# Optimization experiments

Measured on AMD Instinct MI355X. Metric: run time of the kernel, lower is better.

The kernel has to match this reference:

```python
import jax, jax.numpy as jnp
import numpy as np
import math

H = 16
D_MODEL = 1024
D_K = D_MODEL // H
B = 4
S = 2048


def setup_inputs() -> dict:
    key = jax.random.key(0)
    ks = jax.random.split(key, 11)
    s_in = 1.0 / math.sqrt(D_MODEL)
    inp = {
        "query": jax.random.normal(ks[0], (B, S, D_MODEL), dtype=jnp.float32),
        "key_": jax.random.normal(ks[1], (B, S, D_MODEL), dtype=jnp.float32),
        "value": jax.random.normal(ks[2], (B, S, D_MODEL), dtype=jnp.float32),
        # stacked per-head projection weights: [h, d_model, d_k]
        "Wq": jax.random.uniform(ks[3], (H, D_MODEL, D_K), jnp.float32, -s_in, s_in),
        "bq": jax.random.uniform(ks[4], (H, D_K), jnp.float32, -s_in, s_in),
        "Wk": jax.random.uniform(ks[5], (H, D_MODEL, D_K), jnp.float32, -s_in, s_in),
        "bk": jax.random.uniform(ks[6], (H, D_K), jnp.float32, -s_in, s_in),
        "Wv": jax.random.uniform(ks[7], (H, D_MODEL, D_K), jnp.float32, -s_in, s_in),
        "bv": jax.random.uniform(ks[8], (H, D_K), jnp.float32, -s_in, s_in),
        "Wo": jax.random.uniform(ks[9], (D_MODEL, D_MODEL), jnp.float32, -s_in, s_in),
        "bo": jax.random.uniform(ks[10], (D_MODEL,), jnp.float32, -s_in, s_in),
    }
    return inp


def reference(query, key_, value, Wq, bq, Wk, bk, Wv, bv, Wo, bo):
    # Per-head projections, batched over heads: [b,s,m] x [h,m,k] -> [b,h,s,k]
    q = jnp.einsum("bsm,hmk->bhsk", query, Wq) + bq[None, :, None, :]
    k = jnp.einsum("bsm,hmk->bhsk", key_, Wk) + bk[None, :, None, :]
    v = jnp.einsum("bsm,hmk->bhsk", value, Wv) + bv[None, :, None, :]
    # scores: q @ k^T -> [b,h,Sq,Sk]
    scores = jnp.einsum("bhqk,bhsk->bhqs", q, k) / jnp.sqrt(jnp.float32(D_K))
    # NOTE: original code softmaxes over dim=1 of the per-head [N,Sq,Sk]
    # tensor, i.e. the QUERY axis (axis=2 here). Mask has no effect
    # (masked_fill result is discarded in the source), so it is omitted.
    attn = jax.nn.softmax(scores, axis=2)
    ctx = jnp.einsum("bhqs,bhsk->bhqk", attn, v)  # [b,h,Sq,d_k]
    # concat heads along last dim (head-major order matches torch.cat)
    ctx = jnp.transpose(ctx, (0, 2, 1, 3)).reshape(B, S, D_MODEL)
    out = ctx @ Wo.T + bo  # final_W; dropout = identity (eval mode)
    return out
```

## Files before the change

### kernel.cpp

```cpp
#include <hip/hip_runtime.h>


#define DEV __device__ __forceinline__

typedef __bf16 bf16x8 __attribute__((ext_vector_type(8)));
typedef float  f32x4  __attribute__((ext_vector_type(4)));

DEV unsigned short f2bf(float f) {
    __bf16 h = (__bf16)f;
    return __builtin_bit_cast(unsigned short, h);
}

DEV bf16x8 ldfrag(const unsigned short* p) {
    return *reinterpret_cast<const bf16x8*>(p);
}

DEV float fast_exp2(float x) {
#if __has_builtin(__builtin_amdgcn_exp2f)
    return __builtin_amdgcn_exp2f(x);
#else
    return exp2f(x);
#endif
}

DEV void gld16(const unsigned short* g, unsigned short* l) {
    __builtin_amdgcn_global_load_lds(
        (__attribute__((address_space(1))) void*)g,
        (__attribute__((address_space(3))) void*)l, 16, 0, 0);
}

#define MFMA(a,b,c) __builtin_amdgcn_mfma_f32_16x16x32_bf16((a),(b),(c),0,0,0)

#define QSCALE 0.18033688011112042f

__global__ __launch_bounds__(256) void wprep(const float* __restrict__ Wq,
                                             const float* __restrict__ Wk,
                                             const float* __restrict__ Wv,
                                             const float* __restrict__ Wo,
                                             unsigned short* __restrict__ Wt,
                                             unsigned short* __restrict__ Wot) {
    int idx = blockIdx.x * 256 + threadIdx.x;
    int which = blockIdx.y;
    if (which == 3) { Wot[idx] = f2bf(Wo[idx]); return; }
    const float* W = (which == 0) ? Wq : (which == 1) ? Wk : Wv;
    int n = idx >> 10, m = idx & 1023;
    int h = n >> 6, k = n & 63;
    Wt[(size_t)which * 1048576 + idx] = f2bf(W[h * 65536 + m * 64 + k]);
}

__global__ __launch_bounds__(256) void xprep(const float* __restrict__ X,
                                             unsigned short* __restrict__ Xb) {
    int idx = (blockIdx.x * 256 + threadIdx.x) * 4;
    float4 f = *(const float4*)&X[idx];
    ushort4 o;
    o.x = f2bf(f.x); o.y = f2bf(f.y); o.z = f2bf(f.z); o.w = f2bf(f.w);
    *(ushort4*)&Xb[idx] = o;
}

__global__ __launch_bounds__(256) void proj_gemm(
        const unsigned short* __restrict__ Xb, const unsigned short* __restrict__ Bt,
        const float* __restrict__ bias, unsigned short* __restrict__ O,
        unsigned short* __restrict__ Vt, int z) {
    const int tid = threadIdx.x;
    const int bm = blockIdx.x, bn = blockIdx.y;

    __shared__ __align__(16) unsigned short As[128 * 32];
    __shared__ __align__(16) unsigned short Bs[128 * 32];

    const int lane = tid & 63, wid = tid >> 6;
    const int l16 = lane & 15, quad = lane >> 4;
    const int wm = wid & 1, wn = wid >> 1;

    const unsigned short* ga =
        Xb + (size_t)(bm * 128 + wid * 32 + (lane >> 2)) * 1024 + (lane & 3) * 8;
    const unsigned short* gb =
        Bt + (size_t)(bn * 128 + wid * 32 + (lane >> 2)) * 1024 + (lane & 3) * 8;
    unsigned short* la = &As[wid * 32 * 32];
    unsigned short* lb = &Bs[wid * 32 * 32];

    f32x4 acc[4][4] = {};
    for (int kt = 0; kt < 32; ++kt) {
        __syncthreads();
        const int k0 = kt * 32;
        gld16(ga + k0, la);
        gld16(ga + k0 + 16 * 1024, la + 16 * 32);
        gld16(gb + k0, lb);
        gld16(gb + k0 + 16 * 1024, lb + 16 * 32);
        __syncthreads();
        bf16x8 af[4], bfr[4];
#pragma unroll
        for (int mi = 0; mi < 4; ++mi)
            af[mi] = ldfrag(&As[(wm * 64 + mi * 16 + l16) * 32 + quad * 8]);
#pragma unroll
        for (int ni = 0; ni < 4; ++ni)
            bfr[ni] = ldfrag(&Bs[(wn * 64 + ni * 16 + l16) * 32 + quad * 8]);
#pragma unroll
        for (int mi = 0; mi < 4; ++mi)
#pragma unroll
            for (int ni = 0; ni < 4; ++ni)
                acc[mi][ni] = MFMA(af[mi], bfr[ni], acc[mi][ni]);
    }

#pragma unroll
    for (int mi = 0; mi < 4; ++mi)
#pragma unroll
        for (int ni = 0; ni < 4; ++ni)
#pragma unroll
            for (int r = 0; r < 4; ++r) {
                int row = bm * 128 + wm * 64 + mi * 16 + quad * 4 + r;
                int col = bn * 128 + wn * 64 + ni * 16 + l16;
                float v = acc[mi][ni][r] + bias[col];
                if (z == 0) v *= QSCALE;
                int b = row >> 11, s = row & 2047;
                int h = col >> 6, k = col & 63;
                unsigned short o = f2bf(v);
                if (z == 2) {
                    Vt[(size_t)((b * 16 + h) * 64 + k) * 2048 + s] = o;
                } else {
                    O[(size_t)((b * 16 + h) * 2048 + s) * 64 + k] = o;
                }
            }
}

__global__ __launch_bounds__(256) void colsum_vscale(
        const unsigned short* __restrict__ Qh, const unsigned short* __restrict__ Kh,
        unsigned short* __restrict__ Vt) {
    const int tid = threadIdx.x;
    const int st = blockIdx.x, bh = blockIdx.y;
    const unsigned short* Qb = Qh + (size_t)bh * 2048 * 64;
    const unsigned short* Kb = Kh + (size_t)bh * 2048 * 64;

    __shared__ __align__(16) unsigned short Qs[2 * 128 * 32];
    __shared__ float Dtmp[2][128];
    __shared__ float Dsh[128];

    const int lane = tid & 63, wid = tid >> 6;
    const int l16 = lane & 15, quad = lane >> 4;
    const int wm = wid & 1, wn = wid >> 1;

    bf16x8 kf[2][4];
#pragma unroll
    for (int ks = 0; ks < 2; ++ks)
#pragma unroll
        for (int ni = 0; ni < 4; ++ni)
            kf[ks][ni] = ldfrag(&Kb[(size_t)(st * 128 + wn * 64 + ni * 16 + l16) * 64 +
                                    ks * 32 + quad * 8]);

    const unsigned short* gq =
        Qb + (size_t)(wid * 32 + (lane >> 2)) * 64 + (lane & 3) * 8;

    float psum[4] = {0.f, 0.f, 0.f, 0.f};
    for (int q0 = 0; q0 < 2048; q0 += 128) {
        __syncthreads();
#pragma unroll
        for (int ks = 0; ks < 2; ++ks) {
            gld16(gq + (size_t)q0 * 64 + ks * 32, &Qs[ks * 4096 + wid * 32 * 32]);
            gld16(gq + (size_t)(q0 + 16) * 64 + ks * 32,
                  &Qs[ks * 4096 + (wid * 32 + 16) * 32]);
        }
        __syncthreads();
        f32x4 acc[4][4] = {};
#pragma unroll
        for (int ks = 0; ks < 2; ++ks) {
            bf16x8 af[4];
#pragma unroll
            for (int mi = 0; mi < 4; ++mi)
                af[mi] = ldfrag(&Qs[ks * 4096 + (wm * 64 + mi * 16 + l16) * 32 + quad * 8]);
#pragma unroll
            for (int mi = 0; mi < 4; ++mi)
#pragma unroll
                for (int ni = 0; ni < 4; ++ni)
                    acc[mi][ni] = MFMA(af[mi], kf[ks][ni], acc[mi][ni]);
        }
#pragma unroll
        for (int ni = 0; ni < 4; ++ni) {
            float d = 0.f;
#pragma unroll
            for (int mi = 0; mi < 4; ++mi)
#pragma unroll
                for (int r = 0; r < 4; ++r)
                    d += fast_exp2(acc[mi][ni][r]);
            psum[ni] += d;
        }
    }
#pragma unroll
    for (int ni = 0; ni < 4; ++ni) {
        float v = psum[ni];
        v += __shfl_xor(v, 16, 64);
        v += __shfl_xor(v, 32, 64);
        if (quad == 0) Dtmp[wm][wn * 64 + ni * 16 + l16] = v;
    }
    __syncthreads();
    if (tid < 128) Dsh[tid] = 1.0f / (Dtmp[0][tid] + Dtmp[1][tid]);
    __syncthreads();

    const int k = tid >> 2, c = tid & 3;
    unsigned short* vrow = Vt + ((size_t)bh * 64 + k) * 2048 + st * 128 + c * 32;
#pragma unroll
    for (int j = 0; j < 4; ++j) {
        bf16x8 v = *(const bf16x8*)&vrow[j * 8];
        bf16x8 o;
#pragma unroll
        for (int e = 0; e < 8; ++e)
            o[e] = (__bf16)((float)v[e] * Dsh[c * 32 + j * 8 + e]);
        *(bf16x8*)&vrow[j * 8] = o;
    }
}

__global__ __launch_bounds__(256) void attnpv(const unsigned short* __restrict__ Qh,
                                              const unsigned short* __restrict__ Kh,
                                              const unsigned short* __restrict__ Vn,
                                              unsigned short* __restrict__ Ctx) {
    const int tid = threadIdx.x;
    const int qt = blockIdx.x, bh = blockIdx.y;
    const int b = bh >> 4, h = bh & 15;
    const unsigned short* Qb = Qh + (size_t)bh * 2048 * 64;
    const unsigned short* Kb = Kh + (size_t)bh * 2048 * 64;
    const unsigned short* Vb = Vn + (size_t)bh * 64 * 2048;

    __shared__ __align__(16) unsigned short Ps[128 * 72];

    const int lane = tid & 63, wid = tid >> 6;
    const int l16 = lane & 15, quad = lane >> 4;
    const int wq = wid & 1, ws = wid >> 1;

    bf16x8 qf[2][4];
#pragma unroll
    for (int ks = 0; ks < 2; ++ks)
#pragma unroll
        for (int nj = 0; nj < 4; ++nj)
            qf[ks][nj] = ldfrag(&Qb[(size_t)(qt * 128 + wq * 64 + nj * 16 + l16) * 64 +
                                    ks * 32 + quad * 8]);

    const unsigned short* kp = Kb + (size_t)(ws * 32 + l16) * 64 + quad * 8;
    const unsigned short* vp = Vb + (size_t)(ws * 32 + l16) * 2048 + quad * 8;
    unsigned short* psw = &Ps[(size_t)(wq * 64 + l16) * 72 + ws * 32 + quad * 4];
    const unsigned short* psr = &Ps[(size_t)(wq * 64 + l16) * 72 + quad * 8];

    bf16x8 kf[2][2];
#pragma unroll
    for (int mi = 0; mi < 2; ++mi)
#pragma unroll
        for (int ks = 0; ks < 2; ++ks)
            kf[mi][ks] = ldfrag(kp + mi * 1024 + ks * 32);

    f32x4 cacc[2][4] = {};
    for (int s0 = 0; s0 < 2048; s0 += 64) {
        f32x4 sacc[2][4] = {};
#pragma unroll
        for (int ks = 0; ks < 2; ++ks)
#pragma unroll
            for (int mi = 0; mi < 2; ++mi)
#pragma unroll
                for (int nj = 0; nj < 4; ++nj)
                    sacc[mi][nj] = MFMA(kf[mi][ks], qf[ks][nj], sacc[mi][nj]);

        bf16x8 vf[2][2];
#pragma unroll
        for (int mi = 0; mi < 2; ++mi)
#pragma unroll
            for (int ks = 0; ks < 2; ++ks)
                vf[mi][ks] = ldfrag(vp + (size_t)mi * 32768 + ks * 32 + s0);
        const int s1 = (s0 + 64) & 2047;
#pragma unroll
        for (int mi = 0; mi < 2; ++mi)
#pragma unroll
            for (int ks = 0; ks < 2; ++ks)
                kf[mi][ks] = ldfrag(kp + (size_t)s1 * 64 + mi * 1024 + ks * 32);

#pragma unroll
        for (int mi = 0; mi < 2; ++mi)
#pragma unroll
            for (int nj = 0; nj < 4; ++nj) {
                ushort4 p;
                p.x = f2bf(fast_exp2(sacc[mi][nj][0]));
                p.y = f2bf(fast_exp2(sacc[mi][nj][1]));
                p.z = f2bf(fast_exp2(sacc[mi][nj][2]));
                p.w = f2bf(fast_exp2(sacc[mi][nj][3]));
                *(ushort4*)(psw + (size_t)nj * 16 * 72 + mi * 16) = p;
            }
        __syncthreads();

        bf16x8 pf[2][4];
#pragma unroll
        for (int ks2 = 0; ks2 < 2; ++ks2)
#pragma unroll
            for (int nj = 0; nj < 4; ++nj)
                pf[ks2][nj] = ldfrag(psr + (size_t)nj * 16 * 72 + ks2 * 32);
#pragma unroll
        for (int ks2 = 0; ks2 < 2; ++ks2)
#pragma unroll
            for (int mi = 0; mi < 2; ++mi)
#pragma unroll
                for (int nj = 0; nj < 4; ++nj)
                    cacc[mi][nj] = MFMA(vf[mi][ks2], pf[ks2][nj], cacc[mi][nj]);
        __syncthreads();
    }

#pragma unroll
    for (int mi = 0; mi < 2; ++mi)
#pragma unroll
        for (int nj = 0; nj < 4; ++nj) {
            int q = qt * 128 + wq * 64 + nj * 16 + l16;
            int k = ws * 32 + mi * 16 + quad * 4;
            ushort4 o;
            o.x = f2bf(cacc[mi][nj][0]);
            o.y = f2bf(cacc[mi][nj][1]);
            o.z = f2bf(cacc[mi][nj][2]);
            o.w = f2bf(cacc[mi][nj][3]);
            *(ushort4*)&Ctx[(size_t)(b * 2048 + q) * 1024 + h * 64 + k] = o;
        }
}

__global__ __launch_bounds__(256) void out_gemm(const unsigned short* __restrict__ A,
                                                const unsigned short* __restrict__ Bt,
                                                const float* __restrict__ bias,
                                                float* __restrict__ Out) {
    const int tid = threadIdx.x;
    const int bm = blockIdx.x, bn = blockIdx.y;

    __shared__ __align__(16) unsigned short As[128 * 32];
    __shared__ __align__(16) unsigned short Bs[128 * 32];

    const int lane = tid & 63, wid = tid >> 6;
    const int l16 = lane & 15, quad = lane >> 4;
    const int wm = wid & 1, wn = wid >> 1;

    const unsigned short* ga =
        A + (size_t)(bm * 128 + wid * 32 + (lane >> 2)) * 1024 + (lane & 3) * 8;
    const unsigned short* gb =
        Bt + (size_t)(bn * 128 + wid * 32 + (lane >> 2)) * 1024 + (lane & 3) * 8;
    unsigned short* la = &As[wid * 32 * 32];
    unsigned short* lb = &Bs[wid * 32 * 32];

    f32x4 acc[4][4] = {};
    for (int kt = 0; kt < 32; ++kt) {
        __syncthreads();
        const int k0 = kt * 32;
        gld16(ga + k0, la);
        gld16(ga + k0 + 16 * 1024, la + 16 * 32);
        gld16(gb + k0, lb);
        gld16(gb + k0 + 16 * 1024, lb + 16 * 32);
        __syncthreads();
        bf16x8 af[4], bfr[4];
#pragma unroll
        for (int mi = 0; mi < 4; ++mi)
            af[mi] = ldfrag(&As[(wm * 64 + mi * 16 + l16) * 32 + quad * 8]);
#pragma unroll
        for (int ni = 0; ni < 4; ++ni)
            bfr[ni] = ldfrag(&Bs[(wn * 64 + ni * 16 + l16) * 32 + quad * 8]);
#pragma unroll
        for (int mi = 0; mi < 4; ++mi)
#pragma unroll
            for (int ni = 0; ni < 4; ++ni)
                acc[mi][ni] = MFMA(af[mi], bfr[ni], acc[mi][ni]);
    }
#pragma unroll
    for (int mi = 0; mi < 4; ++mi)
#pragma unroll
        for (int ni = 0; ni < 4; ++ni)
#pragma unroll
            for (int r = 0; r < 4; ++r) {
                int row = bm * 128 + wm * 64 + mi * 16 + quad * 4 + r;
                int col = bn * 128 + wn * 64 + ni * 16 + l16;
                Out[(size_t)row * 1024 + col] = acc[mi][ni][r] + bias[col];
            }
}

extern "C" void kernel_launch(void* const* d_in, const int* in_sizes, int n_in,
                              void* d_out, int out_size, void* d_ws, size_t ws_size,
                              hipStream_t stream) {
    (void)in_sizes; (void)n_in; (void)out_size; (void)ws_size;
    const float* X[3] = {(const float*)d_in[0], (const float*)d_in[1],
                         (const float*)d_in[2]};
    const float* Wq = (const float*)d_in[3];
    const float* bq = (const float*)d_in[4];
    const float* Wk = (const float*)d_in[5];
    const float* bk = (const float*)d_in[6];
    const float* Wv = (const float*)d_in[7];
    const float* bv = (const float*)d_in[8];
    const float* Wo = (const float*)d_in[9];
    const float* bo = (const float*)d_in[10];
    const float* bias[3] = {bq, bk, bv};
    float* Out = (float*)d_out;

    char* ws = (char*)d_ws;
    const size_t MB = 1024 * 1024;
    unsigned short* Wt  = (unsigned short*)(ws);
    unsigned short* Wot = (unsigned short*)(ws + 6 * MB);
    unsigned short* Qh  = (unsigned short*)(ws + 8 * MB);
    unsigned short* Kh  = (unsigned short*)(ws + 24 * MB);
    unsigned short* Vt  = (unsigned short*)(ws + 40 * MB);
    unsigned short* Ctx = (unsigned short*)(ws + 56 * MB);
    unsigned short* Xb  = Ctx;
    unsigned short* Oz[3] = {Qh, Kh, Qh };

    wprep<<<dim3(4096, 4), dim3(256), 0, stream>>>(Wq, Wk, Wv, Wo, Wt, Wot);
    for (int z = 0; z < 3; ++z) {
        xprep<<<dim3(8192), dim3(256), 0, stream>>>(X[z], Xb);
        proj_gemm<<<dim3(64, 8), dim3(256), 0, stream>>>(
            Xb, Wt + (size_t)z * 1048576, bias[z], Oz[z], Vt, z);
    }
    colsum_vscale<<<dim3(16, 64), dim3(256), 0, stream>>>(Qh, Kh, Vt);
    attnpv<<<dim3(16, 64), dim3(256), 0, stream>>>(Qh, Kh, Vt, Ctx);
    out_gemm<<<dim3(64, 8), dim3(256), 0, stream>>>(Ctx, Wot, bo, Out);
}
```

Before: 482.4 us.

## Double-buffer Q in colsum and stage K/V through LDS in attnpv

colsum_vscale now double-buffers Q tiles in shared memory, so the next tile's async loads are issued before the current tile's MFMAs and one barrier per iteration is removed. attnpv stops reading K and V fragments straight from global memory into registers. It cooperatively loads them with gld16 into double-buffered LDS, with two warps loading K and two loading V, and prefetches the next tile while the current one computes. The P staging buffer gains an XOR swizzle to cut bank conflicts. This adds LDS traffic and shared-memory footprint, which may reduce occupancy, and it depends on gld16 completion being ordered correctly against the barriers.

Result: faster. 456.6 us (-5.4%).

```diff
diff --git a/kernel.cpp b/kernel.cpp
--- a/kernel.cpp
+++ b/kernel.cpp
@@ -130,7 +130,7 @@
     const unsigned short* Qb = Qh + (size_t)bh * 2048 * 64;
     const unsigned short* Kb = Kh + (size_t)bh * 2048 * 64;
 
-    __shared__ __align__(16) unsigned short Qs[2 * 128 * 32];
+    __shared__ __align__(16) unsigned short Qs[2][2][128 * 32];
     __shared__ float Dtmp[2][128];
     __shared__ float Dsh[128];
 
@@ -149,23 +149,32 @@
     const unsigned short* gq =
         Qb + (size_t)(wid * 32 + (lane >> 2)) * 64 + (lane & 3) * 8;
 
+#pragma unroll
+    for (int ks = 0; ks < 2; ++ks) {
+        gld16(gq + ks * 32, &Qs[0][ks][wid * 32 * 32]);
+        gld16(gq + (size_t)16 * 64 + ks * 32, &Qs[0][ks][(wid * 32 + 16) * 32]);
+    }
+
     float psum[4] = {0.f, 0.f, 0.f, 0.f};
-    for (int q0 = 0; q0 < 2048; q0 += 128) {
-        __syncthreads();
-#pragma unroll
-        for (int ks = 0; ks < 2; ++ks) {
-            gld16(gq + (size_t)q0 * 64 + ks * 32, &Qs[ks * 4096 + wid * 32 * 32]);
-            gld16(gq + (size_t)(q0 + 16) * 64 + ks * 32,
-                  &Qs[ks * 4096 + (wid * 32 + 16) * 32]);
+    for (int it = 0; it < 16; ++it) {
+        const int buf = it & 1;
+        __syncthreads();
+        if (it < 15) {
+            const size_t q1 = (size_t)(it + 1) * 128;
+#pragma unroll
+            for (int ks = 0; ks < 2; ++ks) {
+                gld16(gq + q1 * 64 + ks * 32, &Qs[buf ^ 1][ks][wid * 32 * 32]);
+                gld16(gq + (q1 + 16) * 64 + ks * 32,
+                      &Qs[buf ^ 1][ks][(wid * 32 + 16) * 32]);
+            }
         }
-        __syncthreads();
         f32x4 acc[4][4] = {};
 #pragma unroll
         for (int ks = 0; ks < 2; ++ks) {
             bf16x8 af[4];
 #pragma unroll
             for (int mi = 0; mi < 4; ++mi)
-                af[mi] = ldfrag(&Qs[ks * 4096 + (wm * 64 + mi * 16 + l16) * 32 + quad * 8]);
+                af[mi] = ldfrag(&Qs[buf][ks][(wm * 64 + mi * 16 + l16) * 32 + quad * 8]);
 #pragma unroll
             for (int mi = 0; mi < 4; ++mi)
 #pragma unroll
@@ -218,11 +227,14 @@
     const unsigned short* Kb = Kh + (size_t)bh * 2048 * 64;
     const unsigned short* Vb = Vn + (size_t)bh * 64 * 2048;
 
+    __shared__ __align__(16) unsigned short Ks[2][2][64 * 32];
+    __shared__ __align__(16) unsigned short Vs[2][2][64 * 32];
     __shared__ __align__(16) unsigned short Ps[128 * 72];
 
     const int lane = tid & 63, wid = tid >> 6;
     const int l16 = lane & 15, quad = lane >> 4;
     const int wq = wid & 1, ws = wid >> 1;
+    const int swz = (l16 & 3) << 3;
 
     bf16x8 qf[2][4];
 #pragma unroll
@@ -232,20 +244,32 @@
             qf[ks][nj] = ldfrag(&Qb[(size_t)(qt * 128 + wq * 64 + nj * 16 + l16) * 64 +
                                     ks * 32 + quad * 8]);
 
-    const unsigned short* kp = Kb + (size_t)(ws * 32 + l16) * 64 + quad * 8;
-    const unsigned short* vp = Vb + (size_t)(ws * 32 + l16) * 2048 + quad * 8;
-    unsigned short* psw = &Ps[(size_t)(wq * 64 + l16) * 72 + ws * 32 + quad * 4];
-    const unsigned short* psr = &Ps[(size_t)(wq * 64 + l16) * 72 + quad * 8];
-
-    bf16x8 kf[2][2];
-#pragma unroll
-    for (int mi = 0; mi < 2; ++mi)
-#pragma unroll
-        for (int ks = 0; ks < 2; ++ks)
-            kf[mi][ks] = ldfrag(kp + mi * 1024 + ks * 32);
+    const int srow = lane >> 2, scol = (lane & 3) * 8, half = wid & 1;
+    const unsigned short* gk = Kb + (size_t)srow * 64 + half * 32 + scol;
+    const unsigned short* gv = Vb + (size_t)srow * 2048 + half * 32 + scol;
+
+    if (wid < 2) {
+#pragma unroll
+        for (int gi = 0; gi < 4; ++gi)
+            gld16(gk + (size_t)gi * 16 * 64, &Ks[0][half][gi * 16 * 32]);
+    } else {
+#pragma unroll
+        for (int gi = 0; gi < 4; ++gi)
+            gld16(gv + (size_t)gi * 16 * 2048, &Vs[0][half][gi * 16 * 32]);
+    }
 
     f32x4 cacc[2][4] = {};
-    for (int s0 = 0; s0 < 2048; s0 += 64) {
+    for (int it = 0; it < 32; ++it) {
+        const int buf = it & 1;
+        const int s0 = it * 64;
+        __syncthreads();
+
+        bf16x8 kf[2][2];
+#pragma unroll
+        for (int mi = 0; mi < 2; ++mi)
+#pragma unroll
+            for (int ks = 0; ks < 2; ++ks)
+                kf[mi][ks] = ldfrag(&Ks[buf][ks][(ws * 32 + mi * 16 + l16) * 32 + quad * 8]);
         f32x4 sacc[2][4] = {};
 #pragma unroll
         for (int ks = 0; ks < 2; ++ks)
@@ -254,19 +278,6 @@
 #pragma unroll
                 for (int nj = 0; nj < 4; ++nj)
                     sacc[mi][nj] = MFMA(kf[mi][ks], qf[ks][nj], sacc[mi][nj]);
-
-        bf16x8 vf[2][2];
-#pragma unroll
-        for (int mi = 0; mi < 2; ++mi)
-#pragma unroll
-            for (int ks = 0; ks < 2; ++ks)
-                vf[mi][ks] = ldfrag(vp + (size_t)mi * 32768 + ks * 32 + s0);
-        const int s1 = (s0 + 64) & 2047;
-#pragma unroll
-        for (int mi = 0; mi < 2; ++mi)
-#pragma unroll
-            for (int ks = 0; ks < 2; ++ks)
-                kf[mi][ks] = ldfrag(kp + (size_t)s1 * 64 + mi * 1024 + ks * 32);
 
 #pragma unroll
         for (int mi = 0; mi < 2; ++mi)
@@ -277,16 +288,37 @@
                 p.y = f2bf(fast_exp2(sacc[mi][nj][1]));
                 p.z = f2bf(fast_exp2(sacc[mi][nj][2]));
                 p.w = f2bf(fast_exp2(sacc[mi][nj][3]));
-                *(ushort4*)(psw + (size_t)nj * 16 * 72 + mi * 16) = p;
+                *(ushort4*)&Ps[(size_t)(wq * 64 + nj * 16 + l16) * 72 +
+                               ((ws * 32 + mi * 16 + quad * 4) ^ swz)] = p;
             }
         __syncthreads();
 
-        bf16x8 pf[2][4];
+        if (it < 31) {
+            if (wid < 2) {
+#pragma unroll
+                for (int gi = 0; gi < 4; ++gi)
+                    gld16(gk + (size_t)(s0 + 64 + gi * 16) * 64,
+                          &Ks[buf ^ 1][half][gi * 16 * 32]);
+            } else {
+#pragma unroll
+                for (int gi = 0; gi < 4; ++gi)
+                    gld16(gv + (size_t)(gi * 16) * 2048 + s0 + 64,
+                          &Vs[buf ^ 1][half][gi * 16 * 32]);
+            }
+        }
+
+        bf16x8 vf[2][2], pf[2][4];
+#pragma unroll
+        for (int mi = 0; mi < 2; ++mi)
+#pragma unroll
+            for (int ks2 = 0; ks2 < 2; ++ks2)
+                vf[mi][ks2] = ldfrag(&Vs[buf][ks2][(ws * 32 + mi * 16 + l16) * 32 + quad * 8]);
 #pragma unroll
         for (int ks2 = 0; ks2 < 2; ++ks2)
 #pragma unroll
             for (int nj = 0; nj < 4; ++nj)
-                pf[ks2][nj] = ldfrag(psr + (size_t)nj * 16 * 72 + ks2 * 32);
+                pf[ks2][nj] = ldfrag(&Ps[(size_t)(wq * 64 + nj * 16 + l16) * 72 +
+                                         ((ks2 * 32 + quad * 8) ^ swz)]);
 #pragma unroll
         for (int ks2 = 0; ks2 < 2; ++ks2)
 #pragma unroll
@@ -294,7 +326,6 @@
 #pragma unroll
                 for (int nj = 0; nj < 4; ++nj)
                     cacc[mi][nj] = MFMA(vf[mi][ks2], pf[ks2][nj], cacc[mi][nj]);
-        __syncthreads();
     }
 
 #pragma unroll
```
